# Performance work log

Measured on AMD Instinct MI355X. Metric: run time of the kernel, lower is better.

Reference implementation:

```python
import jax, jax.numpy as jnp
import numpy as np

NEG_INF = -1e9  # stand-in for -INF in masked_fill

def setup_inputs() -> dict:
    key = jax.random.key(0)
    kq, kk, kv, km = jax.random.split(key, 4)
    B, H, S, D = 4, 16, 2048, 128
    query = jax.random.normal(kq, (B, H, S, D), dtype=jnp.float32)
    k_ = jax.random.normal(kk, (B, H, S, D), dtype=jnp.float32)
    value = jax.random.normal(kv, (B, H, S, D), dtype=jnp.float32)
    mask = jax.random.randint(km, (B, 1, 1, S), 0, 2, dtype=jnp.int32)
    return {"query": query, "key": k_, "value": value, "mask": mask}

def reference(query, key, value, mask):
    # _score: dot-product score  [B,H,Sq,Sk]
    score = jnp.einsum("bhqd,bhkd->bhqk", query, key)
    # _probability_normalize: masked_fill(mask==0, -INF) then softmax over keys
    score = jnp.where(mask == 0, NEG_INF, score)
    probability = jax.nn.softmax(score, axis=-1)
    # _attention_aggregate: probability @ value -> [B,H,Sq,D]
    return jnp.einsum("bhqk,bhkd->bhqd", probability, value)
```

## Files before the change

kernel.cpp:

```cpp
#include <hip/hip_runtime.h>

typedef _Float16 f16;
typedef _Float16 f16x8 __attribute__((ext_vector_type(8)));
typedef _Float16 f16x4 __attribute__((ext_vector_type(4)));
typedef float f32x4 __attribute__((ext_vector_type(4)));
typedef float f32x16 __attribute__((ext_vector_type(16)));
typedef unsigned short ushort_t;
typedef unsigned int uint_t;

#define SEQ 2048
#define DIM 128
#define KVBLK 64
#define NTMAX (SEQ / KVBLK)
#define TILE_BYTES 16384

typedef __attribute__((address_space(3))) char lds_char;
typedef __attribute__((address_space(1))) const char glb_char;

__device__ __forceinline__ void gload16(const void* g, void* l) {
  __builtin_amdgcn_global_load_lds((glb_char*)g, (lds_char*)l, 16, 0, 0);
}

__global__ __launch_bounds__(64)
void scan_mask(const int* __restrict__ Mg, int* __restrict__ cidx, int* __restrict__ ncomp) {
  const int b = blockIdx.x;
  const int l = threadIdx.x;
  int m[32];
  int cnt = 0;
  const int* mp = Mg + (size_t)b * SEQ + l * 32;
#pragma unroll
  for (int j = 0; j < 32; ++j) { m[j] = mp[j]; cnt += (m[j] != 0) ? 1 : 0; }
  int inc = cnt;
  for (int ofs = 1; ofs < 64; ofs <<= 1) {
    int v = __shfl_up(inc, ofs);
    if (l >= ofs) inc += v;
  }
  int pos = inc - cnt;
  int* cp = cidx + (size_t)b * SEQ;
  for (int j = 0; j < 32; ++j)
    if (m[j] != 0) cp[pos++] = l * 32 + j;
  if (l == 63) ncomp[b] = inc;
}

__global__ __launch_bounds__(256)
void prep_k(const float* __restrict__ Kg, char* __restrict__ Kws,
            const int* __restrict__ cidx, const int* __restrict__ ncomp) {
  const int tid  = threadIdx.x;
  const int blk  = blockIdx.x;
  const int head = blk >> 5, t = blk & 31;
  const int b    = head >> 4;
  const int nc   = ncomp[b];
  if (t >= ((nc + 63) >> 6)) return;
  const float* hin = Kg + (size_t)head * SEQ * DIM;
  const int* cp = cidx + (size_t)b * SEQ;
  char* out = Kws + (size_t)blk * TILE_BYTES;
#pragma unroll
  for (int i = 0; i < 4; ++i) {
    int u = i * 256 + tid;
    int krow = u >> 4;
    int un   = u & 15;
    int kidx = t * 64 + krow;
    union { f16 h[8]; uint4 u4; } c;
    if (kidx < nc) {
      const float* p = hin + (size_t)cp[kidx] * DIM + un * 8;
      float4 a = *(const float4*)p;
      float4 bq = *(const float4*)(p + 4);
      c.h[0]=(f16)a.x;  c.h[1]=(f16)a.y;  c.h[2]=(f16)a.z;  c.h[3]=(f16)a.w;
      c.h[4]=(f16)bq.x; c.h[5]=(f16)bq.y; c.h[6]=(f16)bq.z; c.h[7]=(f16)bq.w;
    } else {
      c.u4 = uint4{0, 0, 0, 0};
    }
    *(uint4*)(out + krow * 256 + ((un ^ (krow & 15)) << 4)) = c.u4;
  }
}

__global__ __launch_bounds__(256)
void prep_v(const float* __restrict__ Vg, char* __restrict__ Vws,
            const int* __restrict__ cidx, const int* __restrict__ ncomp) {
  __shared__ ushort_t Vs[KVBLK * 133];
  const int tid  = threadIdx.x;
  const int blk  = blockIdx.x;
  const int head = blk >> 5, t = blk & 31;
  const int b    = head >> 4;
  const int nc   = ncomp[b];
  if (t >= ((nc + 63) >> 6)) return;
  const float* hin = Vg + (size_t)head * SEQ * DIM;
  const int* cp = cidx + (size_t)b * SEQ;
  char* out = Vws + (size_t)blk * TILE_BYTES;
#pragma unroll
  for (int i = 0; i < 4; ++i) {
    int u = i * 256 + tid;
    int k  = u >> 4;
    int d0 = (u & 15) * 8;
    int kidx = t * 64 + k;
    f16 h[8];
    if (kidx < nc) {
      const float* p = hin + (size_t)cp[kidx] * DIM + d0;
      float4 a = *(const float4*)p;
      float4 bq = *(const float4*)(p + 4);
      h[0]=(f16)a.x;  h[1]=(f16)a.y;  h[2]=(f16)a.z;  h[3]=(f16)a.w;
      h[4]=(f16)bq.x; h[5]=(f16)bq.y; h[6]=(f16)bq.z; h[7]=(f16)bq.w;
    } else {
#pragma unroll
      for (int j = 0; j < 8; ++j) h[j] = (f16)0.f;
    }
#pragma unroll
    for (int j = 0; j < 8; ++j)
      Vs[k * 133 + d0 + j] = __builtin_bit_cast(ushort_t, h[j]);
  }
  __syncthreads();
#pragma unroll
  for (int i = 0; i < 4; ++i) {
    int u = i * 256 + tid;
    int d  = u >> 3;
    int un = u & 7;
    union { f16 h[8]; uint4 u4; } c;
#pragma unroll
    for (int j = 0; j < 8; ++j)
      c.h[j] = __builtin_bit_cast(f16, Vs[(un * 8 + j) * 133 + d]);
    *(uint4*)(out + d * 128 + ((un ^ (d & 7)) << 4)) = c.u4;
  }
}

__device__ __forceinline__ void build_paf(const uint_t pkA[2][4], const uint_t pkB[2][4],
                                          f16x8 paf[4], int h) {
#pragma unroll
  for (int ks = 0; ks < 4; ++ks) {
    const int sk = ks & 1, tt = ks >> 1;
    uint_t Ao = h ? pkA[tt][2 * sk + 1] : pkA[tt][2 * sk];
    uint_t Bo = h ? pkB[tt][2 * sk + 1] : pkB[tt][2 * sk];
    uint_t As = h ? pkA[tt][2 * sk]     : pkA[tt][2 * sk + 1];
    uint_t Bs = h ? pkB[tt][2 * sk]     : pkB[tt][2 * sk + 1];
    uint_t Ax = (uint_t)__shfl_xor((int)As, 32);
    uint_t Bx = (uint_t)__shfl_xor((int)Bs, 32);
    union { uint_t u[4]; f16x8 v; } pa;
    pa.u[0] = h ? Ax : Ao;
    pa.u[1] = h ? Bx : Bo;
    pa.u[2] = h ? Ao : Ax;
    pa.u[3] = h ? Bo : Bx;
    paf[ks] = pa.v;
  }
}

__device__ __forceinline__ void pv_mfma(const char* __restrict__ Vbuf,
                                        const f16x8 paf[4], f32x16 oacc[4],
                                        int q32, int h) {
  __builtin_amdgcn_s_setprio(1);
#pragma unroll
  for (int ks = 0; ks < 4; ++ks) {
#pragma unroll
    for (int dvt = 0; dvt < 4; ++dvt) {
      const int dv = dvt * 32 + q32;
      f16x8 vf = *(const f16x8*)(&Vbuf[dv * 128 + (((2 * ks + h) ^ (dv & 7)) << 4)]);
      oacc[dvt] = __builtin_amdgcn_mfma_f32_32x32x16_f16(vf, paf[ks], oacc[dvt], 0, 0, 0);
    }
  }
  __builtin_amdgcn_s_setprio(0);
}

__global__ __launch_bounds__(512, 2)
void attn_main32(const float* __restrict__ Qg, const char* __restrict__ Kws,
                 const char* __restrict__ Vws, const int* __restrict__ ncomp,
                 float* __restrict__ Og) {
  __shared__ __align__(16) char Kb[2][TILE_BYTES];
  __shared__ __align__(16) char Vb[2][TILE_BYTES];

  const int tid  = threadIdx.x;
  const int lane = tid & 63;
  const int q32  = lane & 31;
  const int h    = lane >> 5;

  const int bid  = blockIdx.x;
  const int head = (bid & 7) * 8 + (bid >> 6);
  const int qblk = (bid >> 3) & 7;
  const size_t hbase = (size_t)head * SEQ * DIM;
  const int bb = head >> 4;

  const int nc  = ncomp[bb];
  const int ntb = (nc + 63) >> 6;

  const char* ktb = Kws + ((size_t)(head * NTMAX) << 14);
  const char* vtb = Vws + ((size_t)(head * NTMAX) << 14);

  const int qrow = qblk * 256 + (tid >> 6) * 32 + q32;

  f16x8 qf[8];
  {
    const float* qp = Qg + hbase + (size_t)qrow * DIM + h * 8;
#pragma unroll
    for (int c = 0; c < 8; ++c) {
      float4 a = *(const float4*)(qp + c * 16);
      float4 b = *(const float4*)(qp + c * 16 + 4);
      f16x8 f;
      f[0]=(f16)a.x; f[1]=(f16)a.y; f[2]=(f16)a.z; f[3]=(f16)a.w;
      f[4]=(f16)b.x; f[5]=(f16)b.y; f[6]=(f16)b.z; f[7]=(f16)b.w;
      qf[c] = f;
    }
  }

  f32x16 oacc[4];
#pragma unroll
  for (int dvt = 0; dvt < 4; ++dvt) oacc[dvt] = (f32x16)(0.f);
  float mrow = -INFINITY, lrow = 0.f;

  uint_t pkPA[2][4], pkPB[2][4];
#pragma unroll
  for (int t2 = 0; t2 < 2; ++t2)
#pragma unroll
    for (int m = 0; m < 4; ++m) { pkPA[t2][m] = 0; pkPB[t2][m] = 0; }

#pragma unroll
  for (int i = 0; i < 2; ++i) {
    int u = i * 512 + tid;
    gload16(ktb + u * 16, &Kb[0][u * 16]);
  }

  int cur = 0;
  for (int t = 0; t < ntb; ++t) {
    {
      const int tn = (t + 1 == ntb) ? 0 : t + 1;
      const char* kt2 = ktb + ((size_t)tn << 14);
      const char* vt2 = vtb + ((size_t)t << 14);
      const int nb = cur ^ 1;
#pragma unroll
      for (int i = 0; i < 2; ++i) {
        int u = i * 512 + tid;
        gload16(kt2 + u * 16, &Kb[nb][u * 16]);
      }
#pragma unroll
      for (int i = 0; i < 2; ++i) {
        int u = i * 512 + tid;
        gload16(vt2 + u * 16, &Vb[cur][u * 16]);
      }
    }
    asm volatile("s_waitcnt vmcnt(4)" ::: "memory");
    __builtin_amdgcn_s_barrier();
    asm volatile("" ::: "memory");

    f32x16 s0, s1;
    {
      const int kb0 = t * 64;
      if (kb0 + 32 <= nc) {
        s0 = (f32x16)(0.f);
      } else {
#pragma unroll
        for (int ri = 0; ri < 16; ++ri)
          s0[ri] = (kb0 + (ri >> 2) * 8 + 4 * h + (ri & 3) < nc) ? 0.f : -1e9f;
      }
      const int kb1 = t * 64 + 32;
      if (kb1 + 32 <= nc) {
        s1 = (f32x16)(0.f);
      } else {
#pragma unroll
        for (int ri = 0; ri < 16; ++ri)
          s1[ri] = (kb1 + (ri >> 2) * 8 + 4 * h + (ri & 3) < nc) ? 0.f : -1e9f;
      }
      const int kr0 = q32,      sw0 = kr0 & 15;
      const int kr1 = 32 + q32, sw1 = kr1 & 15;
      __builtin_amdgcn_s_setprio(1);
#pragma unroll
      for (int c = 0; c < 8; ++c) {
        f16x8 k0 = *(const f16x8*)(&Kb[cur][kr0 * 256 + (((2 * c + h) ^ sw0) << 4)]);
        s0 = __builtin_amdgcn_mfma_f32_32x32x16_f16(k0, qf[c], s0, 0, 0, 0);
        f16x8 k1 = *(const f16x8*)(&Kb[cur][kr1 * 256 + (((2 * c + h) ^ sw1) << 4)]);
        s1 = __builtin_amdgcn_mfma_f32_32x32x16_f16(k1, qf[c], s1, 0, 0, 0);
      }
      __builtin_amdgcn_s_setprio(0);
    }

    if (t > 0) {
      f16x8 paf[4];
      build_paf(pkPA, pkPB, paf, h);
      pv_mfma(&Vb[cur ^ 1][0], paf, oacc, q32, h);
    }

    {
      float mx[16];
#pragma unroll
      for (int r = 0; r < 16; ++r) mx[r] = fmaxf(s0[r], s1[r]);
#pragma unroll
      for (int r = 0; r < 8; ++r) mx[r] = fmaxf(mx[r], mx[r + 8]);
#pragma unroll
      for (int r = 0; r < 4; ++r) mx[r] = fmaxf(mx[r], mx[r + 4]);
      float pmax = fmaxf(fmaxf(mx[0], mx[1]), fmaxf(mx[2], mx[3]));
      pmax = fmaxf(pmax, __shfl_xor(pmax, 32));

      if (!__all(pmax - mrow <= 8.f)) {
        float mnew = fmaxf(mrow, pmax);
        float scf = __expf(mrow - mnew);
#pragma unroll
        for (int dvt = 0; dvt < 4; ++dvt)
#pragma unroll
          for (int r = 0; r < 16; ++r) oacc[dvt][r] *= scf;
        lrow *= scf;
        mrow = mnew;
      }

      float ps[16];
#pragma unroll
      for (int r = 0; r < 16; ++r) {
        s0[r] = __expf(s0[r] - mrow);
        s1[r] = __expf(s1[r] - mrow);
        ps[r] = s0[r] + s1[r];
      }
#pragma unroll
      for (int r = 0; r < 8; ++r) ps[r] += ps[r + 8];
#pragma unroll
      for (int r = 0; r < 4; ++r) ps[r] += ps[r + 4];
      float psum = (ps[0] + ps[1]) + (ps[2] + ps[3]);
      psum += __shfl_xor(psum, 32);
      lrow += psum;

#pragma unroll
      for (int m = 0; m < 4; ++m) {
        pkPA[0][m] = __builtin_bit_cast(uint_t,
            __builtin_amdgcn_cvt_pkrtz(s0[4 * m + 0], s0[4 * m + 1]));
        pkPB[0][m] = __builtin_bit_cast(uint_t,
            __builtin_amdgcn_cvt_pkrtz(s0[4 * m + 2], s0[4 * m + 3]));
        pkPA[1][m] = __builtin_bit_cast(uint_t,
            __builtin_amdgcn_cvt_pkrtz(s1[4 * m + 0], s1[4 * m + 1]));
        pkPB[1][m] = __builtin_bit_cast(uint_t,
            __builtin_amdgcn_cvt_pkrtz(s1[4 * m + 2], s1[4 * m + 3]));
      }
    }

    asm volatile("" ::: "memory");
    __builtin_amdgcn_s_barrier();
    asm volatile("" ::: "memory");
    cur ^= 1;
  }

  asm volatile("s_waitcnt vmcnt(0)" ::: "memory");
  __builtin_amdgcn_s_barrier();
  asm volatile("" ::: "memory");
  if (ntb > 0) {
    f16x8 paf[4];
    build_paf(pkPA, pkPB, paf, h);
    pv_mfma(&Vb[cur ^ 1][0], paf, oacc, q32, h);
  }

  const float inv = 1.0f / lrow;
  float* op = Og + hbase + (size_t)qrow * DIM;
#pragma unroll
  for (int dvt = 0; dvt < 4; ++dvt)
#pragma unroll
    for (int rq = 0; rq < 4; ++rq) {
      float4 o4;
      o4.x = oacc[dvt][4 * rq + 0] * inv;
      o4.y = oacc[dvt][4 * rq + 1] * inv;
      o4.z = oacc[dvt][4 * rq + 2] * inv;
      o4.w = oacc[dvt][4 * rq + 3] * inv;
      *(float4*)(op + dvt * 32 + rq * 8 + h * 4) = o4;
    }
}

#define QT 64
#define P_STRIDE 72
#define VT_STRIDE 76
typedef _Float16 f16x4_t __attribute__((ext_vector_type(4)));
__global__ __launch_bounds__(256, 2)
void attn_fwd_fb(const float* __restrict__ Qg, const float* __restrict__ Kg,
                 const float* __restrict__ Vg, const int* __restrict__ Mg,
                 float* __restrict__ Og) {
  __shared__ __align__(16) ushort_t K_lds[QT * DIM];
  __shared__ __align__(16) ushort_t Vt_lds[DIM * VT_STRIDE];
  __shared__ __align__(16) ushort_t P_lds[QT * P_STRIDE];
  __shared__ int M_lds[KVBLK];
  const int tid  = threadIdx.x;
  const int lane = tid & 63;
  const int w    = tid >> 6;
  const int li   = lane & 15;
  const int g    = lane >> 4;
  const int bid  = blockIdx.x;
  const int nid  = (bid & 7) * 256 + (bid >> 3);
  const int head = nid >> 5;
  const int qblk = nid & 31;
  const size_t hbase = (size_t)head * SEQ * DIM;
  const int bb = head >> 4;
  f16x8 qf[4];
  {
    const float* qp = Qg + hbase + (size_t)(qblk * QT + w * 16 + li) * DIM + g * 8;
#pragma unroll
    for (int d0 = 0; d0 < 4; ++d0) {
      float4 a = *(const float4*)(qp + d0 * 32);
      float4 b = *(const float4*)(qp + d0 * 32 + 4);
      f16x8 f;
      f[0]=(f16)a.x; f[1]=(f16)a.y; f[2]=(f16)a.z; f[3]=(f16)a.w;
      f[4]=(f16)b.x; f[5]=(f16)b.y; f[6]=(f16)b.z; f[7]=(f16)b.w;
      qf[d0] = f;
    }
  }
  float mrow[4], lrow[4];
  f32x4 oacc[8];
#pragma unroll
  for (int r = 0; r < 4; ++r) { mrow[r] = -INFINITY; lrow[r] = 0.f; }
#pragma unroll
  for (int dt = 0; dt < 8; ++dt) oacc[dt] = (f32x4)(0.f);
  for (int t = 0; t < NTMAX; ++t) {
    const int k0 = t * KVBLK;
    __syncthreads();
    {
      const float4* kgp = (const float4*)(Kg + hbase + (size_t)k0 * DIM);
#pragma unroll
      for (int rr = 0; rr < 8; ++rr) {
        int fi = rr * 256 + tid;
        int krow = fi >> 5;
        int d4 = fi & 31;
        float4 v = kgp[fi];
        union { f16 h[4]; uint2 u; } c;
        c.h[0]=(f16)v.x; c.h[1]=(f16)v.y; c.h[2]=(f16)v.z; c.h[3]=(f16)v.w;
        int off = krow * 256 + ((d4 * 8) ^ ((krow & 7) << 4));
        *(uint2*)((char*)K_lds + off) = c.u;
      }
    }
    {
      const float* vgp = Vg + hbase + (size_t)k0 * DIM;
#pragma unroll
      for (int rr = 0; rr < 16; ++rr) {
        int u = rr * 256 + tid;
        int d = u & 127;
        int k2 = (u >> 7) * 2;
        float v0 = vgp[(size_t)k2 * DIM + d];
        float v1 = vgp[(size_t)(k2 + 1) * DIM + d];
        union { f16 h[2]; unsigned int u32; } c;
        c.h[0]=(f16)v0; c.h[1]=(f16)v1;
        *(unsigned int*)(Vt_lds + d * VT_STRIDE + k2) = c.u32;
      }
    }
    if (tid < KVBLK) M_lds[tid] = Mg[(size_t)bb * SEQ + k0 + tid];
    __syncthreads();
    f32x4 sacc[4];
#pragma unroll
    for (int kt = 0; kt < 4; ++kt) sacc[kt] = (f32x4)(0.f);
#pragma unroll
    for (int kt = 0; kt < 4; ++kt) {
      const int krow = kt * 16 + li;
      const int swz = (krow & 7) << 4;
#pragma unroll
      for (int d0 = 0; d0 < 4; ++d0) {
        f16x8 kf = *(const f16x8*)((const char*)K_lds + krow * 256 + ((d0 * 64 + g * 16) ^ swz));
        sacc[kt] = __builtin_amdgcn_mfma_f32_16x16x32_f16(qf[d0], kf, sacc[kt], 0, 0, 0);
      }
    }
    float tmax[4] = {-INFINITY, -INFINITY, -INFINITY, -INFINITY};
#pragma unroll
    for (int kt = 0; kt < 4; ++kt) {
      const bool ok = (M_lds[kt * 16 + li] != 0);
#pragma unroll
      for (int r = 0; r < 4; ++r) {
        float sv = ok ? sacc[kt][r] : -1e9f;
        sacc[kt][r] = sv;
        tmax[r] = fmaxf(tmax[r], sv);
      }
    }
#pragma unroll
    for (int r = 0; r < 4; ++r) {
      tmax[r] = fmaxf(tmax[r], __shfl_xor(tmax[r], 1));
      tmax[r] = fmaxf(tmax[r], __shfl_xor(tmax[r], 2));
      tmax[r] = fmaxf(tmax[r], __shfl_xor(tmax[r], 4));
      tmax[r] = fmaxf(tmax[r], __shfl_xor(tmax[r], 8));
    }
    float sc[4], psum[4];
#pragma unroll
    for (int r = 0; r < 4; ++r) {
      float mnew = fmaxf(mrow[r], tmax[r]);
      sc[r] = __expf(mrow[r] - mnew);
      mrow[r] = mnew;
      psum[r] = 0.f;
    }
#pragma unroll
    for (int dt = 0; dt < 8; ++dt)
#pragma unroll
      for (int r = 0; r < 4; ++r) oacc[dt][r] *= sc[r];
#pragma unroll
    for (int kt = 0; kt < 4; ++kt) {
#pragma unroll
      for (int r = 0; r < 4; ++r) {
        float p = __expf(sacc[kt][r] - mrow[r]);
        psum[r] += p;
        P_lds[(w * 16 + g * 4 + r) * P_STRIDE + kt * 16 + li] =
            __builtin_bit_cast(ushort_t, (f16)p);
      }
    }
#pragma unroll
    for (int r = 0; r < 4; ++r) {
      psum[r] += __shfl_xor(psum[r], 1);
      psum[r] += __shfl_xor(psum[r], 2);
      psum[r] += __shfl_xor(psum[r], 4);
      psum[r] += __shfl_xor(psum[r], 8);
      lrow[r] = lrow[r] * sc[r] + psum[r];
    }
#pragma unroll
    for (int c = 0; c < 2; ++c) {
      f16x8 pa = *(const f16x8*)(P_lds + (w * 16 + li) * P_STRIDE + c * 32 + g * 8);
#pragma unroll
      for (int dt = 0; dt < 8; ++dt) {
        const ushort_t* vp = Vt_lds + (dt * 16 + li) * VT_STRIDE + c * 32 + g * 8;
        f16x4_t v0 = *(const f16x4_t*)vp;
        f16x4_t v1 = *(const f16x4_t*)(vp + 4);
        f16x8 vf;
        vf[0]=v0[0]; vf[1]=v0[1]; vf[2]=v0[2]; vf[3]=v0[3];
        vf[4]=v1[0]; vf[5]=v1[1]; vf[6]=v1[2]; vf[7]=v1[3];
        oacc[dt] = __builtin_amdgcn_mfma_f32_16x16x32_f16(pa, vf, oacc[dt], 0, 0, 0);
      }
    }
  }
#pragma unroll
  for (int r = 0; r < 4; ++r) {
    float inv = 1.0f / lrow[r];
    float* op = Og + hbase + (size_t)(qblk * QT + w * 16 + g * 4 + r) * DIM + li;
#pragma unroll
    for (int dt = 0; dt < 8; ++dt) op[dt * 16] = oacc[dt][r] * inv;
  }
}

extern "C" void kernel_launch(void* const* d_in, const int* in_sizes, int n_in,
                              void* d_out, int out_size, void* d_ws, size_t ws_size,
                              hipStream_t stream) {
  (void)in_sizes; (void)n_in; (void)out_size;
  const float* Q = (const float*)d_in[0];
  const float* K = (const float*)d_in[1];
  const float* V = (const float*)d_in[2];
  const int*   M = (const int*)d_in[3];
  float*       O = (float*)d_out;

  const size_t half = (size_t)2048 * TILE_BYTES;
  const size_t cidx_off  = 2 * half;
  const size_t ncomp_off = cidx_off + (size_t)4 * SEQ * sizeof(int);
  const size_t need = ncomp_off + 4 * sizeof(int);

  if (ws_size >= need) {
    char* Kws = (char*)d_ws;
    char* Vws = Kws + half;
    int*  cidx  = (int*)((char*)d_ws + cidx_off);
    int*  ncomp = (int*)((char*)d_ws + ncomp_off);
    scan_mask<<<dim3(4), dim3(64), 0, stream>>>(M, cidx, ncomp);
    prep_k<<<dim3(2048), dim3(256), 0, stream>>>(K, Kws, cidx, ncomp);
    prep_v<<<dim3(2048), dim3(256), 0, stream>>>(V, Vws, cidx, ncomp);
    attn_main32<<<dim3(512), dim3(512), 0, stream>>>(Q, Kws, Vws, ncomp, O);
  } else {
    attn_fwd_fb<<<dim3(2048), dim3(256), 0, stream>>>(Q, K, V, M, O);
  }
}
```

Measured before the change: 138.5 us.

## Interleave QK and PV MFMAs, peel first tile, stage Q via LDS with exp2

The first KV tile is peeled out of the main loop, so the steady-state loop always runs the PV product for the previous tile. That PV work is now interleaved MFMA-by-MFMA with the current tile's QK MFMAs, instead of being a separate phase, to keep the matrix units busy and hide LDS latency. Q is loaded with coalesced float4 reads, pre-scaled by log2(e), converted to fp16 and transposed through swizzled LDS. This lets the softmax use exp2f, with the rescale threshold adjusted to match the log2 domain. The loop is unrolled by two and the max reduction is reshaped; the interleaving raises register pressure and the peel assumes at least one valid tile.

```diff
diff --git a/kernel.cpp b/kernel.cpp
--- a/kernel.cpp
+++ b/kernel.cpp
@@ -13,6 +13,7 @@
 #define KVBLK 64
 #define NTMAX (SEQ / KVBLK)
 #define TILE_BYTES 16384
+#define LOG2E 1.44269504f
 
 typedef __attribute__((address_space(3))) char lds_char;
 typedef __attribute__((address_space(1))) const char glb_char;
@@ -142,33 +143,19 @@
   }
 }
 
-__device__ __forceinline__ void pv_mfma(const char* __restrict__ Vbuf,
-                                        const f16x8 paf[4], f32x16 oacc[4],
-                                        int q32, int h) {
-  __builtin_amdgcn_s_setprio(1);
-#pragma unroll
-  for (int ks = 0; ks < 4; ++ks) {
-#pragma unroll
-    for (int dvt = 0; dvt < 4; ++dvt) {
-      const int dv = dvt * 32 + q32;
-      f16x8 vf = *(const f16x8*)(&Vbuf[dv * 128 + (((2 * ks + h) ^ (dv & 7)) << 4)]);
-      oacc[dvt] = __builtin_amdgcn_mfma_f32_32x32x16_f16(vf, paf[ks], oacc[dvt], 0, 0, 0);
-    }
-  }
-  __builtin_amdgcn_s_setprio(0);
-}
-
 __global__ __launch_bounds__(512, 2)
 void attn_main32(const float* __restrict__ Qg, const char* __restrict__ Kws,
                  const char* __restrict__ Vws, const int* __restrict__ ncomp,
                  float* __restrict__ Og) {
-  __shared__ __align__(16) char Kb[2][TILE_BYTES];
-  __shared__ __align__(16) char Vb[2][TILE_BYTES];
+  __shared__ __align__(16) char smem[65536];
+#define KBUF(b) (smem + (b) * TILE_BYTES)
+#define VBUF(b) (smem + 32768 + (b) * TILE_BYTES)
 
   const int tid  = threadIdx.x;
   const int lane = tid & 63;
   const int q32  = lane & 31;
   const int h    = lane >> 5;
+  const int w    = tid >> 6;
 
   const int bid  = blockIdx.x;
   const int head = (bid & 7) * 8 + (bid >> 6);
@@ -182,55 +169,128 @@
   const char* ktb = Kws + ((size_t)(head * NTMAX) << 14);
   const char* vtb = Vws + ((size_t)(head * NTMAX) << 14);
 
-  const int qrow = qblk * 256 + (tid >> 6) * 32 + q32;
+  const int qrow = qblk * 256 + w * 32 + q32;
 
   f16x8 qf[8];
   {
-    const float* qp = Qg + hbase + (size_t)qrow * DIM + h * 8;
-#pragma unroll
-    for (int c = 0; c < 8; ++c) {
-      float4 a = *(const float4*)(qp + c * 16);
-      float4 b = *(const float4*)(qp + c * 16 + 4);
-      f16x8 f;
-      f[0]=(f16)a.x; f[1]=(f16)a.y; f[2]=(f16)a.z; f[3]=(f16)a.w;
-      f[4]=(f16)b.x; f[5]=(f16)b.y; f[6]=(f16)b.z; f[7]=(f16)b.w;
-      qf[c] = f;
-    }
-  }
+    char* qsl = smem + w * 8192;
+    const float* qsrc = Qg + hbase + (size_t)(qblk * 256 + w * 32) * DIM;
+#pragma unroll
+    for (int hf = 0; hf < 2; ++hf) {
+      float4 qv[8];
+#pragma unroll
+      for (int i = 0; i < 8; ++i)
+        qv[i] = *(const float4*)(qsrc + (size_t)((hf * 8 + i) * 64 + lane) * 4);
+#pragma unroll
+      for (int i = 0; i < 8; ++i) {
+        int idx = (hf * 8 + i) * 64 + lane;
+        int r   = idx >> 5;
+        int d0  = (idx & 31) * 4;
+        uint2 wv;
+        wv.x = __builtin_bit_cast(uint_t,
+            __builtin_amdgcn_cvt_pkrtz(qv[i].x * LOG2E, qv[i].y * LOG2E));
+        wv.y = __builtin_bit_cast(uint_t,
+            __builtin_amdgcn_cvt_pkrtz(qv[i].z * LOG2E, qv[i].w * LOG2E));
+        *(uint2*)(qsl + r * 256 + (((d0 >> 3) ^ (r & 15)) << 4) + (d0 & 7) * 2) = wv;
+      }
+    }
+#pragma unroll
+    for (int c = 0; c < 8; ++c)
+      qf[c] = *(const f16x8*)(qsl + q32 * 256 + (((2 * c + h) ^ (q32 & 15)) << 4));
+  }
+  __syncthreads();
 
   f32x16 oacc[4];
 #pragma unroll
   for (int dvt = 0; dvt < 4; ++dvt) oacc[dvt] = (f32x16)(0.f);
   float mrow = -INFINITY, lrow = 0.f;
-
   uint_t pkPA[2][4], pkPB[2][4];
-#pragma unroll
-  for (int t2 = 0; t2 < 2; ++t2)
-#pragma unroll
-    for (int m = 0; m < 4; ++m) { pkPA[t2][m] = 0; pkPB[t2][m] = 0; }
 
 #pragma unroll
   for (int i = 0; i < 2; ++i) {
     int u = i * 512 + tid;
-    gload16(ktb + u * 16, &Kb[0][u * 16]);
-  }
-
-  int cur = 0;
-  for (int t = 0; t < ntb; ++t) {
+    gload16(ktb + u * 16, KBUF(0) + u * 16);
+  }
+
+  {
+    const char* kt2 = ktb + ((size_t)((ntb > 1) ? 1 : 0) << 14);
+#pragma unroll
+    for (int i = 0; i < 2; ++i) {
+      int u = i * 512 + tid;
+      gload16(kt2 + u * 16, KBUF(1) + u * 16);
+      gload16(vtb + u * 16, VBUF(0) + u * 16);
+    }
+    asm volatile("s_waitcnt vmcnt(4)" ::: "memory");
+    __builtin_amdgcn_s_barrier();
+    asm volatile("" ::: "memory");
+
+    f32x16 s0, s1;
+    if (64 <= nc) { s0 = (f32x16)(0.f); s1 = (f32x16)(0.f); }
+    else {
+#pragma unroll
+      for (int ri = 0; ri < 16; ++ri) {
+        s0[ri] = ((ri >> 2) * 8 + 4 * h + (ri & 3) < nc) ? 0.f : -1e9f;
+        s1[ri] = (32 + (ri >> 2) * 8 + 4 * h + (ri & 3) < nc) ? 0.f : -1e9f;
+      }
+    }
+    const int kr0 = q32, sw0 = kr0 & 15;
+    const int kr1 = 32 + q32, sw1 = kr1 & 15;
+    __builtin_amdgcn_s_setprio(1);
+#pragma unroll
+    for (int c = 0; c < 8; ++c) {
+      f16x8 k0 = *(const f16x8*)(KBUF(0) + kr0 * 256 + (((2 * c + h) ^ sw0) << 4));
+      s0 = __builtin_amdgcn_mfma_f32_32x32x16_f16(k0, qf[c], s0, 0, 0, 0);
+      f16x8 k1 = *(const f16x8*)(KBUF(0) + kr1 * 256 + (((2 * c + h) ^ sw1) << 4));
+      s1 = __builtin_amdgcn_mfma_f32_32x32x16_f16(k1, qf[c], s1, 0, 0, 0);
+    }
+    __builtin_amdgcn_s_setprio(0);
+
+    float mx[16];
+#pragma unroll
+    for (int r = 0; r < 16; ++r) mx[r] = fmaxf(s0[r], s1[r]);
+#pragma unroll
+    for (int r = 0; r < 5; ++r) mx[r] = fmaxf(fmaxf(mx[r], mx[r + 5]), mx[r + 10]);
+    float pmax = fmaxf(fmaxf(fmaxf(mx[0], mx[1]), fmaxf(mx[2], mx[3])), fmaxf(mx[4], mx[15]));
+    pmax = fmaxf(pmax, __shfl_xor(pmax, 32));
+    mrow = pmax;
+    float ps[16];
+#pragma unroll
+    for (int r = 0; r < 16; ++r) {
+      s0[r] = exp2f(s0[r] - mrow);
+      s1[r] = exp2f(s1[r] - mrow);
+      ps[r] = s0[r] + s1[r];
+    }
+#pragma unroll
+    for (int r = 0; r < 8; ++r) ps[r] += ps[r + 8];
+#pragma unroll
+    for (int r = 0; r < 4; ++r) ps[r] += ps[r + 4];
+    float psum = (ps[0] + ps[1]) + (ps[2] + ps[3]);
+    psum += __shfl_xor(psum, 32);
+    lrow += psum;
+#pragma unroll
+    for (int m = 0; m < 4; ++m) {
+      pkPA[0][m] = __builtin_bit_cast(uint_t, __builtin_amdgcn_cvt_pkrtz(s0[4*m+0], s0[4*m+1]));
+      pkPB[0][m] = __builtin_bit_cast(uint_t, __builtin_amdgcn_cvt_pkrtz(s0[4*m+2], s0[4*m+3]));
+      pkPA[1][m] = __builtin_bit_cast(uint_t, __builtin_amdgcn_cvt_pkrtz(s1[4*m+0], s1[4*m+1]));
+      pkPB[1][m] = __builtin_bit_cast(uint_t, __builtin_amdgcn_cvt_pkrtz(s1[4*m+2], s1[4*m+3]));
+    }
+    asm volatile("" ::: "memory");
+    __builtin_amdgcn_s_barrier();
+    asm volatile("" ::: "memory");
+  }
+
+  int cur = 1;
+#pragma unroll 2
+  for (int t = 1; t < ntb; ++t) {
     {
       const int tn = (t + 1 == ntb) ? 0 : t + 1;
       const char* kt2 = ktb + ((size_t)tn << 14);
       const char* vt2 = vtb + ((size_t)t << 14);
-      const int nb = cur ^ 1;
 #pragma unroll
       for (int i = 0; i < 2; ++i) {
         int u = i * 512 + tid;
-        gload16(kt2 + u * 16, &Kb[nb][u * 16]);
-      }
-#pragma unroll
-      for (int i = 0; i < 2; ++i) {
-        int u = i * 512 + tid;
-        gload16(vt2 + u * 16, &Vb[cur][u * 16]);
+        gload16(kt2 + u * 16, KBUF(cur ^ 1) + u * 16);
+        gload16(vt2 + u * 16, VBUF(cur) + u * 16);
       }
     }
     asm volatile("s_waitcnt vmcnt(4)" ::: "memory");
@@ -239,55 +299,57 @@
 
     f32x16 s0, s1;
     {
-      const int kb0 = t * 64;
-      if (kb0 + 32 <= nc) {
-        s0 = (f32x16)(0.f);
-      } else {
-#pragma unroll
-        for (int ri = 0; ri < 16; ++ri)
+      const int kb0 = t * 64, kb1 = t * 64 + 32;
+      if (kb1 + 32 <= nc) { s0 = (f32x16)(0.f); s1 = (f32x16)(0.f); }
+      else {
+#pragma unroll
+        for (int ri = 0; ri < 16; ++ri) {
           s0[ri] = (kb0 + (ri >> 2) * 8 + 4 * h + (ri & 3) < nc) ? 0.f : -1e9f;
-      }
-      const int kb1 = t * 64 + 32;
-      if (kb1 + 32 <= nc) {
-        s1 = (f32x16)(0.f);
-      } else {
-#pragma unroll
-        for (int ri = 0; ri < 16; ++ri)
           s1[ri] = (kb1 + (ri >> 2) * 8 + 4 * h + (ri & 3) < nc) ? 0.f : -1e9f;
-      }
-      const int kr0 = q32,      sw0 = kr0 & 15;
-      const int kr1 = 32 + q32, sw1 = kr1 & 15;
-      __builtin_amdgcn_s_setprio(1);
-#pragma unroll
-      for (int c = 0; c < 8; ++c) {
-        f16x8 k0 = *(const f16x8*)(&Kb[cur][kr0 * 256 + (((2 * c + h) ^ sw0) << 4)]);
-        s0 = __builtin_amdgcn_mfma_f32_32x32x16_f16(k0, qf[c], s0, 0, 0, 0);
-        f16x8 k1 = *(const f16x8*)(&Kb[cur][kr1 * 256 + (((2 * c + h) ^ sw1) << 4)]);
-        s1 = __builtin_amdgcn_mfma_f32_32x32x16_f16(k1, qf[c], s1, 0, 0, 0);
-      }
-      __builtin_amdgcn_s_setprio(0);
-    }
-
-    if (t > 0) {
-      f16x8 paf[4];
-      build_paf(pkPA, pkPB, paf, h);
-      pv_mfma(&Vb[cur ^ 1][0], paf, oacc, q32, h);
-    }
+        }
+      }
+    }
+    f16x8 paf[4];
+    build_paf(pkPA, pkPB, paf, h);
+
+    const char* kb = KBUF(cur);
+    const char* vb = VBUF(cur ^ 1);
+    const int kr0 = q32, sw0 = kr0 & 15;
+    const int kr1 = 32 + q32, sw1 = kr1 & 15;
+    __builtin_amdgcn_s_setprio(1);
+#pragma unroll
+    for (int c = 0; c < 8; ++c) {
+      const int ksA = (2 * c) >> 2,     dvA = (2 * c) & 3;
+      const int ksB = (2 * c + 1) >> 2, dvB = (2 * c + 1) & 3;
+      f16x8 k0 = *(const f16x8*)(kb + kr0 * 256 + (((2 * c + h) ^ sw0) << 4));
+      s0 = __builtin_amdgcn_mfma_f32_32x32x16_f16(k0, qf[c], s0, 0, 0, 0);
+      {
+        const int dv = dvA * 32 + q32;
+        f16x8 vf = *(const f16x8*)(vb + dv * 128 + (((2 * ksA + h) ^ (dv & 7)) << 4));
+        oacc[dvA] = __builtin_amdgcn_mfma_f32_32x32x16_f16(vf, paf[ksA], oacc[dvA], 0, 0, 0);
+      }
+      f16x8 k1 = *(const f16x8*)(kb + kr1 * 256 + (((2 * c + h) ^ sw1) << 4));
+      s1 = __builtin_amdgcn_mfma_f32_32x32x16_f16(k1, qf[c], s1, 0, 0, 0);
+      {
+        const int dv = dvB * 32 + q32;
+        f16x8 vf = *(const f16x8*)(vb + dv * 128 + (((2 * ksB + h) ^ (dv & 7)) << 4));
+        oacc[dvB] = __builtin_amdgcn_mfma_f32_32x32x16_f16(vf, paf[ksB], oacc[dvB], 0, 0, 0);
+      }
+    }
+    __builtin_amdgcn_s_setprio(0);
 
     {
       float mx[16];
 #pragma unroll
       for (int r = 0; r < 16; ++r) mx[r] = fmaxf(s0[r], s1[r]);
 #pragma unroll
-      for (int r = 0; r < 8; ++r) mx[r] = fmaxf(mx[r], mx[r + 8]);
-#pragma unroll
-      for (int r = 0; r < 4; ++r) mx[r] = fmaxf(mx[r], mx[r + 4]);
-      float pmax = fmaxf(fmaxf(mx[0], mx[1]), fmaxf(mx[2], mx[3]));
+      for (int r = 0; r < 5; ++r) mx[r] = fmaxf(fmaxf(mx[r], mx[r + 5]), mx[r + 10]);
+      float pmax = fmaxf(fmaxf(fmaxf(mx[0], mx[1]), fmaxf(mx[2], mx[3])), fmaxf(mx[4], mx[15]));
       pmax = fmaxf(pmax, __shfl_xor(pmax, 32));
 
-      if (!__all(pmax - mrow <= 8.f)) {
+      if (!__all(pmax - mrow <= 11.6f)) {
         float mnew = fmaxf(mrow, pmax);
-        float scf = __expf(mrow - mnew);
+        float scf = exp2f(mrow - mnew);
 #pragma unroll
         for (int dvt = 0; dvt < 4; ++dvt)
 #pragma unroll
@@ -295,12 +357,11 @@
         lrow *= scf;
         mrow = mnew;
       }
-
       float ps[16];
 #pragma unroll
       for (int r = 0; r < 16; ++r) {
-        s0[r] = __expf(s0[r] - mrow);
-        s1[r] = __expf(s1[r] - mrow);
+        s0[r] = exp2f(s0[r] - mrow);
+        s1[r] = exp2f(s1[r] - mrow);
         ps[r] = s0[r] + s1[r];
       }
 #pragma unroll
@@ -310,20 +371,14 @@
       float psum = (ps[0] + ps[1]) + (ps[2] + ps[3]);
       psum += __shfl_xor(psum, 32);
       lrow += psum;
-
 #pragma unroll
       for (int m = 0; m < 4; ++m) {
-        pkPA[0][m] = __builtin_bit_cast(uint_t,
-            __builtin_amdgcn_cvt_pkrtz(s0[4 * m + 0], s0[4 * m + 1]));
-        pkPB[0][m] = __builtin_bit_cast(uint_t,
-            __builtin_amdgcn_cvt_pkrtz(s0[4 * m + 2], s0[4 * m + 3]));
-        pkPA[1][m] = __builtin_bit_cast(uint_t,
-            __builtin_amdgcn_cvt_pkrtz(s1[4 * m + 0], s1[4 * m + 1]));
-        pkPB[1][m] = __builtin_bit_cast(uint_t,
-            __builtin_amdgcn_cvt_pkrtz(s1[4 * m + 2], s1[4 * m + 3]));
-      }
-    }
-
+        pkPA[0][m] = __builtin_bit_cast(uint_t, __builtin_amdgcn_cvt_pkrtz(s0[4*m+0], s0[4*m+1]));
+        pkPB[0][m] = __builtin_bit_cast(uint_t, __builtin_amdgcn_cvt_pkrtz(s0[4*m+2], s0[4*m+3]));
+        pkPA[1][m] = __builtin_bit_cast(uint_t, __builtin_amdgcn_cvt_pkrtz(s1[4*m+0], s1[4*m+1]));
+        pkPB[1][m] = __builtin_bit_cast(uint_t, __builtin_amdgcn_cvt_pkrtz(s1[4*m+2], s1[4*m+3]));
+      }
+    }
     asm volatile("" ::: "memory");
     __builtin_amdgcn_s_barrier();
     asm volatile("" ::: "memory");
@@ -333,10 +388,20 @@
   asm volatile("s_waitcnt vmcnt(0)" ::: "memory");
   __builtin_amdgcn_s_barrier();
   asm volatile("" ::: "memory");
-  if (ntb > 0) {
+  {
     f16x8 paf[4];
     build_paf(pkPA, pkPB, paf, h);
-    pv_mfma(&Vb[cur ^ 1][0], paf, oacc, q32, h);
+    const char* vb = VBUF(cur ^ 1);
+    __builtin_amdgcn_s_setprio(1);
+#pragma unroll
+    for (int ks = 0; ks < 4; ++ks)
+#pragma unroll
+      for (int dvt = 0; dvt < 4; ++dvt) {
+        const int dv = dvt * 32 + q32;
+        f16x8 vf = *(const f16x8*)(vb + dv * 128 + (((2 * ks + h) ^ (dv & 7)) << 4));
+        oacc[dvt] = __builtin_amdgcn_mfma_f32_32x32x16_f16(vf, paf[ks], oacc[dvt], 0, 0, 0);
+      }
+    __builtin_amdgcn_s_setprio(0);
   }
 
   const float inv = 1.0f / lrow;
@@ -352,6 +417,8 @@
       o4.w = oacc[dvt][4 * rq + 3] * inv;
       *(float4*)(op + dvt * 32 + rq * 8 + h * 4) = o4;
     }
+#undef KBUF
+#undef VBUF
 }
 
 #define QT 64
```

Measured after the change: 156.2 us. +12.7%, slower.

## Use 1024-thread blocks covering 512 query rows to halve K/V tile loads

Applied to the files above, without the earlier changes.

The attention kernel now launches 256 blocks of 1024 threads, each handling 512 query rows of one head instead of 256. Each K/V tile staged in LDS is reused by twice as many waves, so each thread issues one async load per tile and global K/V traffic per head is halved. In exchange, occupancy drops to one block per CU with a larger barrier scope, and the grid shrinks to 256 blocks on a device with many CUs, which may leave compute units idle. The ntb>0 guard on the final PV step was also removed.

```diff
diff --git a/kernel.cpp b/kernel.cpp
--- a/kernel.cpp
+++ b/kernel.cpp
@@ -158,7 +158,7 @@
   __builtin_amdgcn_s_setprio(0);
 }
 
-__global__ __launch_bounds__(512, 2)
+__global__ __launch_bounds__(1024, 1)
 void attn_main32(const float* __restrict__ Qg, const char* __restrict__ Kws,
                  const char* __restrict__ Vws, const int* __restrict__ ncomp,
                  float* __restrict__ Og) {
@@ -169,10 +169,12 @@
   const int lane = tid & 63;
   const int q32  = lane & 31;
   const int h    = lane >> 5;
+  const int w    = tid >> 6;
 
   const int bid  = blockIdx.x;
-  const int head = (bid & 7) * 8 + (bid >> 6);
-  const int qblk = (bid >> 3) & 7;
+  const int nid  = (bid & 7) * 32 + (bid >> 3);
+  const int head = nid >> 2;
+  const int qblk = nid & 3;
   const size_t hbase = (size_t)head * SEQ * DIM;
   const int bb = head >> 4;
 
@@ -182,7 +184,7 @@
   const char* ktb = Kws + ((size_t)(head * NTMAX) << 14);
   const char* vtb = Vws + ((size_t)(head * NTMAX) << 14);
 
-  const int qrow = qblk * 256 + (tid >> 6) * 32 + q32;
+  const int qrow = qblk * 512 + w * 32 + q32;
 
   f16x8 qf[8];
   {
@@ -209,31 +211,16 @@
 #pragma unroll
     for (int m = 0; m < 4; ++m) { pkPA[t2][m] = 0; pkPB[t2][m] = 0; }
 
-#pragma unroll
-  for (int i = 0; i < 2; ++i) {
-    int u = i * 512 + tid;
-    gload16(ktb + u * 16, &Kb[0][u * 16]);
-  }
+  gload16(ktb + tid * 16, &Kb[0][tid * 16]);
 
   int cur = 0;
   for (int t = 0; t < ntb; ++t) {
     {
       const int tn = (t + 1 == ntb) ? 0 : t + 1;
-      const char* kt2 = ktb + ((size_t)tn << 14);
-      const char* vt2 = vtb + ((size_t)t << 14);
-      const int nb = cur ^ 1;
-#pragma unroll
-      for (int i = 0; i < 2; ++i) {
-        int u = i * 512 + tid;
-        gload16(kt2 + u * 16, &Kb[nb][u * 16]);
-      }
-#pragma unroll
-      for (int i = 0; i < 2; ++i) {
-        int u = i * 512 + tid;
-        gload16(vt2 + u * 16, &Vb[cur][u * 16]);
-      }
-    }
-    asm volatile("s_waitcnt vmcnt(4)" ::: "memory");
+      gload16(ktb + ((size_t)tn << 14) + tid * 16, &Kb[cur ^ 1][tid * 16]);
+      gload16(vtb + ((size_t)t << 14) + tid * 16, &Vb[cur][tid * 16]);
+    }
+    asm volatile("s_waitcnt vmcnt(2)" ::: "memory");
     __builtin_amdgcn_s_barrier();
     asm volatile("" ::: "memory");
 
@@ -333,7 +320,7 @@
   asm volatile("s_waitcnt vmcnt(0)" ::: "memory");
   __builtin_amdgcn_s_barrier();
   asm volatile("" ::: "memory");
-  if (ntb > 0) {
+  {
     f16x8 paf[4];
     build_paf(pkPA, pkPB, paf, h);
     pv_mfma(&Vb[cur ^ 1][0], paf, oacc, q32, h);
@@ -537,7 +524,7 @@
     scan_mask<<<dim3(4), dim3(64), 0, stream>>>(M, cidx, ncomp);
     prep_k<<<dim3(2048), dim3(256), 0, stream>>>(K, Kws, cidx, ncomp);
     prep_v<<<dim3(2048), dim3(256), 0, stream>>>(V, Vws, cidx, ncomp);
-    attn_main32<<<dim3(512), dim3(512), 0, stream>>>(Q, Kws, Vws, ncomp, O);
+    attn_main32<<<dim3(256), dim3(1024), 0, stream>>>(Q, Kws, Vws, ncomp, O);
   } else {
     attn_fwd_fb<<<dim3(2048), dim3(256), 0, stream>>>(Q, K, V, M, O);
   }
```

After: 240.7 us. +73.7%, slower.
